# Performance work log

Measured on AMD Instinct MI355X. Metric: run time of the kernel, lower is better.

The kernel has to match this reference:

```python
import jax, jax.numpy as jnp
import numpy as np

RING_SIZE = 4
SEGMENT_LEN = 1024
DILATION_RATE = 2
EPS = 1e-8


def setup_inputs() -> dict:
    key = jax.random.key(0)
    kq, kk, kv = jax.random.split(key, 3)
    shape = (1, 4096, 16, 64)  # (b, n, h, d)
    q = jax.random.normal(kq, shape, dtype=jnp.float32)
    k = jax.random.normal(kk, shape, dtype=jnp.float32)
    v = jax.random.normal(kv, shape, dtype=jnp.float32)
    return {"q": q, "k": k, "v": v}


def _gather_dilated_chunks(k_local, v_local, chunk_size):
    """Replicate the ring loop: rank 0, dist not initialized -> KV chunk is
    always the local chunk; only the dilation offset varies per ring step.
    Returns concatenated dilated K, V of total length ring_size*chunk_size."""
    ks, vs = [], []
    base = jnp.arange(chunk_size)
    for step in range(RING_SIZE):
        chunk_rank = (-step) % RING_SIZE
        chunk_start = chunk_rank * chunk_size
        offset = (chunk_start // SEGMENT_LEN) % DILATION_RATE
        if DILATION_RATE == 1:
            idx = base
        else:
            idx = (base * DILATION_RATE + offset) % chunk_size
        ks.append(k_local[:, idx])
        vs.append(v_local[:, idx])
    return jnp.concatenate(ks, axis=1), jnp.concatenate(vs, axis=1)


def reference(q, k, v):
    b, n, h, d = q.shape
    chunk_size = n // RING_SIZE
    k_local = k[:, :chunk_size]  # rank 0 local chunk
    v_local = v[:, :chunk_size]
    K, V = _gather_dilated_chunks(k_local, v_local, chunk_size)  # (b, n, h, d)

    # Online softmax over ring steps is mathematically a single stable softmax
    # over the concatenation of all chunk scores, with +1e-8 on sum_exp.
    scale = 1.0 / jnp.sqrt(jnp.asarray(d, dtype=q.dtype))
    scores = jnp.einsum("bqhd,bkhd->bhqk", q, K) * scale  # (b, h, n, n)
    m = jnp.max(scores, axis=-1, keepdims=True)
    p = jnp.exp(scores - m)
    denom = jnp.sum(p, axis=-1, keepdims=True) + EPS  # (b, h, q, 1)
    out = jnp.einsum("bhqk,bkhd->bqhd", p, V)  # (b, q, h, d)
    out = out / jnp.transpose(denom, (0, 2, 1, 3))  # -> (b, q, h, 1)
    return out
```

## Files before the change

kernel.cpp:

```cpp
#include <hip/hip_runtime.h>


typedef __attribute__((ext_vector_type(8))) _Float16 f16x8;
typedef __attribute__((ext_vector_type(4))) float    f32x4;

constexpr int HEADS = 16;
constexpr int NQ    = 4096;
constexpr int NK    = 1024;
constexpr int KB    = 64;
constexpr int NT    = NK / KB;
constexpr int NTW   = NT / 2;

constexpr int IMG_K  = 0;
constexpr int IMG_V  = 8192;
constexpr int IMG_SZ = 16384;

__device__ __forceinline__ int swz(int row, int b) {
    return row * 128 + (b ^ ((row & 7) << 4));
}

__global__ __launch_bounds__(256)
void prepass(const float* __restrict__ kg, const float* __restrict__ vg,
             char* __restrict__ ws)
{
    const int kt = blockIdx.x;
    const int h  = blockIdx.y;
    const int kb = kt * KB;
    char* img = ws + (size_t)(h * NT + kt) * IMG_SZ;
    const int tid = threadIdx.x;

    #pragma unroll
    for (int i = 0; i < 2; ++i) {
        int u = i * 256 + tid;
        int f = u >> 6, l = u & 63;
        int t = f >> 1, cc = f & 1;
        int g = l >> 4, c = l & 15;
        const float* src = kg + (size_t)(kb + 16 * t + c) * 1024 + h * 64 + 32 * cc + 8 * g;
        float4 a = *(const float4*)src;
        float4 b = *(const float4*)(src + 4);
        f16x8 kk;
        kk[0] = (_Float16)(a.x * 0.125f); kk[1] = (_Float16)(a.y * 0.125f);
        kk[2] = (_Float16)(a.z * 0.125f); kk[3] = (_Float16)(a.w * 0.125f);
        kk[4] = (_Float16)(b.x * 0.125f); kk[5] = (_Float16)(b.y * 0.125f);
        kk[6] = (_Float16)(b.z * 0.125f); kk[7] = (_Float16)(b.w * 0.125f);
        *(f16x8*)(img + IMG_K + u * 16) = kk;
    }

    #pragma unroll
    for (int i = 0; i < 2; ++i) {
        int u = i * 256 + tid;
        int f = u >> 6, l = u & 63;
        int cc = f >> 2, td = f & 3;
        int g = l >> 4, c = l & 15;
        f16x8 vv;
        #pragma unroll
        for (int e = 0; e < 8; ++e)
            vv[e] = (_Float16)vg[(size_t)(kb + cc * 32 + g * 8 + e) * 1024 + h * 64 + td * 16 + c];
        *(f16x8*)(img + IMG_V + u * 16) = vv;
    }
}

__global__ __launch_bounds__(128, 2)
void ring_attn_v14(const float* __restrict__ qg,
                   const char* __restrict__ ws,
                   float* __restrict__ outg)
{
    __shared__ char  Pl[2][8192];
    __shared__ float Ob[64][64];
    __shared__ float Ls[64];

    const int bid  = blockIdx.x;
    const int xcd  = bid & 7;
    const int slot = bid >> 3;
    const int h    = xcd * 2 + (slot >> 6);
    const int qw   = slot & 63;

    const int tid  = threadIdx.x;
    const int w    = tid >> 6;
    const int lane = tid & 63;
    const int g    = lane >> 4;
    const int c    = lane & 15;
    const int qbase = qw * 64;

    const int rot  = ((bid >> 3) ^ (w << 2)) & 7;

    f16x8 qf[4][2];
    #pragma unroll
    for (int H = 0; H < 4; ++H)
        #pragma unroll
        for (int cc = 0; cc < 2; ++cc) {
            const float* src = qg + (size_t)(qbase + 16 * H + c) * 1024 + h * 64 + 32 * cc + 8 * g;
            float4 a = *(const float4*)src;
            float4 b = *(const float4*)(src + 4);
            f16x8 qq;
            qq[0] = (_Float16)a.x; qq[1] = (_Float16)a.y;
            qq[2] = (_Float16)a.z; qq[3] = (_Float16)a.w;
            qq[4] = (_Float16)b.x; qq[5] = (_Float16)b.y;
            qq[6] = (_Float16)b.z; qq[7] = (_Float16)b.w;
            qf[H][cc] = qq;
        }

    const f32x4 zero4 = {0.f, 0.f, 0.f, 0.f};

    f32x4 o[4][4];
    #pragma unroll
    for (int H = 0; H < 4; ++H)
        #pragma unroll
        for (int td = 0; td < 4; ++td) o[H][td] = zero4;
    float lac[4] = {0.f, 0.f, 0.f, 0.f};

    const char* himg = ws + (size_t)h * NT * IMG_SZ + lane * 16;
    char* pbuf = Pl[w];

    #pragma unroll 1
    for (int i = 0; i < NTW; ++i) {
        const int kt = w * NTW + ((i + rot) & 7);
        const char* img = himg + (size_t)kt * IMG_SZ;

        f16x8 kv[8];
        #pragma unroll
        for (int f = 0; f < 8; ++f)
            kv[f] = *(const f16x8*)(img + IMG_K + f * 1024);

        f32x4 s0[4], s1[4], s2[4], s3[4];
        __builtin_amdgcn_s_setprio(1);
        #pragma unroll
        for (int t = 0; t < 4; ++t) {
            s0[t] = __builtin_amdgcn_mfma_f32_16x16x32_f16(kv[2 * t],     qf[0][0], zero4, 0, 0, 0);
            s0[t] = __builtin_amdgcn_mfma_f32_16x16x32_f16(kv[2 * t + 1], qf[0][1], s0[t], 0, 0, 0);
            s1[t] = __builtin_amdgcn_mfma_f32_16x16x32_f16(kv[2 * t],     qf[1][0], zero4, 0, 0, 0);
            s1[t] = __builtin_amdgcn_mfma_f32_16x16x32_f16(kv[2 * t + 1], qf[1][1], s1[t], 0, 0, 0);
        }
        __builtin_amdgcn_s_setprio(0);
        #pragma unroll
        for (int t = 0; t < 4; ++t) {
            float p0 = __builtin_amdgcn_exp2f(fmaf(s0[t][0], 1.44269504f, -2.88539008f));
            float p1 = __builtin_amdgcn_exp2f(fmaf(s0[t][1], 1.44269504f, -2.88539008f));
            float p2 = __builtin_amdgcn_exp2f(fmaf(s0[t][2], 1.44269504f, -2.88539008f));
            float p3 = __builtin_amdgcn_exp2f(fmaf(s0[t][3], 1.44269504f, -2.88539008f));
            lac[0] += (p0 + p1) + (p2 + p3);
            auto lo = __builtin_amdgcn_cvt_pkrtz(p0, p1);
            auto hi = __builtin_amdgcn_cvt_pkrtz(p2, p3);
            uint2 pk;
            pk.x = __builtin_bit_cast(unsigned int, lo);
            pk.y = __builtin_bit_cast(unsigned int, hi);
            *(uint2*)(pbuf + swz(c, 32 * t + 8 * g)) = pk;
        }
        #pragma unroll
        for (int t = 0; t < 4; ++t) {
            float p0 = __builtin_amdgcn_exp2f(fmaf(s1[t][0], 1.44269504f, -2.88539008f));
            float p1 = __builtin_amdgcn_exp2f(fmaf(s1[t][1], 1.44269504f, -2.88539008f));
            float p2 = __builtin_amdgcn_exp2f(fmaf(s1[t][2], 1.44269504f, -2.88539008f));
            float p3 = __builtin_amdgcn_exp2f(fmaf(s1[t][3], 1.44269504f, -2.88539008f));
            lac[1] += (p0 + p1) + (p2 + p3);
            auto lo = __builtin_amdgcn_cvt_pkrtz(p0, p1);
            auto hi = __builtin_amdgcn_cvt_pkrtz(p2, p3);
            uint2 pk;
            pk.x = __builtin_bit_cast(unsigned int, lo);
            pk.y = __builtin_bit_cast(unsigned int, hi);
            *(uint2*)(pbuf + swz(16 + c, 32 * t + 8 * g)) = pk;
        }

        __builtin_amdgcn_s_setprio(1);
        #pragma unroll
        for (int t = 0; t < 4; ++t) {
            s2[t] = __builtin_amdgcn_mfma_f32_16x16x32_f16(kv[2 * t],     qf[2][0], zero4, 0, 0, 0);
            s2[t] = __builtin_amdgcn_mfma_f32_16x16x32_f16(kv[2 * t + 1], qf[2][1], s2[t], 0, 0, 0);
            s3[t] = __builtin_amdgcn_mfma_f32_16x16x32_f16(kv[2 * t],     qf[3][0], zero4, 0, 0, 0);
            s3[t] = __builtin_amdgcn_mfma_f32_16x16x32_f16(kv[2 * t + 1], qf[3][1], s3[t], 0, 0, 0);
        }
        __builtin_amdgcn_s_setprio(0);

        #pragma unroll
        for (int f = 0; f < 8; ++f)
            kv[f] = *(const f16x8*)(img + IMG_V + f * 1024);

        #pragma unroll
        for (int t = 0; t < 4; ++t) {
            float p0 = __builtin_amdgcn_exp2f(fmaf(s2[t][0], 1.44269504f, -2.88539008f));
            float p1 = __builtin_amdgcn_exp2f(fmaf(s2[t][1], 1.44269504f, -2.88539008f));
            float p2 = __builtin_amdgcn_exp2f(fmaf(s2[t][2], 1.44269504f, -2.88539008f));
            float p3 = __builtin_amdgcn_exp2f(fmaf(s2[t][3], 1.44269504f, -2.88539008f));
            lac[2] += (p0 + p1) + (p2 + p3);
            auto lo = __builtin_amdgcn_cvt_pkrtz(p0, p1);
            auto hi = __builtin_amdgcn_cvt_pkrtz(p2, p3);
            uint2 pk;
            pk.x = __builtin_bit_cast(unsigned int, lo);
            pk.y = __builtin_bit_cast(unsigned int, hi);
            *(uint2*)(pbuf + swz(32 + c, 32 * t + 8 * g)) = pk;
        }
        #pragma unroll
        for (int t = 0; t < 4; ++t) {
            float p0 = __builtin_amdgcn_exp2f(fmaf(s3[t][0], 1.44269504f, -2.88539008f));
            float p1 = __builtin_amdgcn_exp2f(fmaf(s3[t][1], 1.44269504f, -2.88539008f));
            float p2 = __builtin_amdgcn_exp2f(fmaf(s3[t][2], 1.44269504f, -2.88539008f));
            float p3 = __builtin_amdgcn_exp2f(fmaf(s3[t][3], 1.44269504f, -2.88539008f));
            lac[3] += (p0 + p1) + (p2 + p3);
            auto lo = __builtin_amdgcn_cvt_pkrtz(p0, p1);
            auto hi = __builtin_amdgcn_cvt_pkrtz(p2, p3);
            uint2 pk;
            pk.x = __builtin_bit_cast(unsigned int, lo);
            pk.y = __builtin_bit_cast(unsigned int, hi);
            *(uint2*)(pbuf + swz(48 + c, 32 * t + 8 * g)) = pk;
        }

        __builtin_amdgcn_s_setprio(1);
        #pragma unroll
        for (int cc = 0; cc < 2; ++cc) {
            #pragma unroll
            for (int H = 0; H < 4; ++H) {
                f16x8 pa = *(const f16x8*)(pbuf + swz(16 * H + c, 64 * cc + 16 * g));
                #pragma unroll
                for (int td = 0; td < 4; ++td)
                    o[H][td] = __builtin_amdgcn_mfma_f32_16x16x32_f16(pa, kv[cc * 4 + td], o[H][td], 0, 0, 0);
            }
        }
        __builtin_amdgcn_s_setprio(0);
        __builtin_amdgcn_sched_barrier(0);
    }

    #pragma unroll
    for (int H = 0; H < 4; ++H) {
        lac[H] += __shfl_xor(lac[H], 16);
        lac[H] += __shfl_xor(lac[H], 32);
    }

    if (w == 1) {
        #pragma unroll
        for (int H = 0; H < 4; ++H)
            #pragma unroll
            for (int td = 0; td < 4; ++td)
                #pragma unroll
                for (int r = 0; r < 4; ++r)
                    Ob[16 * H + 4 * g + r][16 * td + c] = o[H][td][r];
        if (lane < 16) {
            #pragma unroll
            for (int H = 0; H < 4; ++H) Ls[16 * H + lane] = lac[H];
        }
    }
    __syncthreads();

    if (w == 0) {
        #pragma unroll
        for (int H = 0; H < 4; ++H) {
            #pragma unroll
            for (int r = 0; r < 4; ++r) {
                int q2  = 16 * H + 4 * g + r;
                float lq = __shfl(lac[H], 4 * g + r) + Ls[q2];
                float inv = 1.f / lq;
                int qrow = qbase + q2;
                #pragma unroll
                for (int td = 0; td < 4; ++td)
                    outg[(size_t)qrow * 1024 + h * 64 + 16 * td + c] =
                        (o[H][td][r] + Ob[q2][16 * td + c]) * inv;
            }
        }
    }
}

extern "C" void kernel_launch(void* const* d_in, const int* in_sizes, int n_in,
                              void* d_out, int out_size, void* d_ws, size_t ws_size,
                              hipStream_t stream) {
    const float* q = (const float*)d_in[0];
    const float* k = (const float*)d_in[1];
    const float* v = (const float*)d_in[2];
    float* out = (float*)d_out;
    char* ws = (char*)d_ws;

    prepass<<<dim3(NT, HEADS), dim3(256), 0, stream>>>(k, v, ws);
    ring_attn_v14<<<dim3(1024), dim3(128), 0, stream>>>(q, ws, out);
}
```

Measured before the change: 37.20 us.

## Feed P directly from registers into PV MFMA by transposing the product

New measurement: 34.84 us. 6.3% less time.

```diff
diff --git a/kernel.cpp b/kernel.cpp
--- a/kernel.cpp
+++ b/kernel.cpp
@@ -3,6 +3,7 @@
 
 typedef __attribute__((ext_vector_type(8))) _Float16 f16x8;
 typedef __attribute__((ext_vector_type(4))) float    f32x4;
+typedef __attribute__((ext_vector_type(4))) int      i32x4;
 
 constexpr int HEADS = 16;
 constexpr int NQ    = 4096;
@@ -50,24 +51,24 @@
     for (int i = 0; i < 2; ++i) {
         int u = i * 256 + tid;
         int f = u >> 6, l = u & 63;
-        int cc = f >> 2, td = f & 3;
+        int m = f >> 2, td = f & 3;
         int g = l >> 4, c = l & 15;
         f16x8 vv;
         #pragma unroll
-        for (int e = 0; e < 8; ++e)
-            vv[e] = (_Float16)vg[(size_t)(kb + cc * 32 + g * 8 + e) * 1024 + h * 64 + td * 16 + c];
+        for (int e = 0; e < 8; ++e) {
+            int key = kb + 32 * m + 16 * (e >> 2) + 4 * g + (e & 3);
+            vv[e] = (_Float16)vg[(size_t)key * 1024 + h * 64 + 16 * td + c];
+        }
         *(f16x8*)(img + IMG_V + u * 16) = vv;
     }
 }
 
 __global__ __launch_bounds__(128, 2)
-void ring_attn_v14(const float* __restrict__ qg,
+void ring_attn_v15(const float* __restrict__ qg,
                    const char* __restrict__ ws,
                    float* __restrict__ outg)
 {
-    __shared__ char  Pl[2][8192];
-    __shared__ float Ob[64][64];
-    __shared__ float Ls[64];
+    __shared__ __align__(16) float Ob[64 * 68 + 64];
 
     const int bid  = blockIdx.x;
     const int xcd  = bid & 7;
@@ -110,7 +111,6 @@
     float lac[4] = {0.f, 0.f, 0.f, 0.f};
 
     const char* himg = ws + (size_t)h * NT * IMG_SZ + lane * 16;
-    char* pbuf = Pl[w];
 
     #pragma unroll 1
     for (int i = 0; i < NTW; ++i) {
@@ -123,6 +123,7 @@
             kv[f] = *(const f16x8*)(img + IMG_K + f * 1024);
 
         f32x4 s0[4], s1[4], s2[4], s3[4];
+        unsigned int wv[4][4][2];
         __builtin_amdgcn_s_setprio(1);
         #pragma unroll
         for (int t = 0; t < 4; ++t) {
@@ -139,12 +140,8 @@
             float p2 = __builtin_amdgcn_exp2f(fmaf(s0[t][2], 1.44269504f, -2.88539008f));
             float p3 = __builtin_amdgcn_exp2f(fmaf(s0[t][3], 1.44269504f, -2.88539008f));
             lac[0] += (p0 + p1) + (p2 + p3);
-            auto lo = __builtin_amdgcn_cvt_pkrtz(p0, p1);
-            auto hi = __builtin_amdgcn_cvt_pkrtz(p2, p3);
-            uint2 pk;
-            pk.x = __builtin_bit_cast(unsigned int, lo);
-            pk.y = __builtin_bit_cast(unsigned int, hi);
-            *(uint2*)(pbuf + swz(c, 32 * t + 8 * g)) = pk;
+            wv[0][t][0] = __builtin_bit_cast(unsigned int, __builtin_amdgcn_cvt_pkrtz(p0, p1));
+            wv[0][t][1] = __builtin_bit_cast(unsigned int, __builtin_amdgcn_cvt_pkrtz(p2, p3));
         }
         #pragma unroll
         for (int t = 0; t < 4; ++t) {
@@ -153,12 +150,8 @@
             float p2 = __builtin_amdgcn_exp2f(fmaf(s1[t][2], 1.44269504f, -2.88539008f));
             float p3 = __builtin_amdgcn_exp2f(fmaf(s1[t][3], 1.44269504f, -2.88539008f));
             lac[1] += (p0 + p1) + (p2 + p3);
-            auto lo = __builtin_amdgcn_cvt_pkrtz(p0, p1);
-            auto hi = __builtin_amdgcn_cvt_pkrtz(p2, p3);
-            uint2 pk;
-            pk.x = __builtin_bit_cast(unsigned int, lo);
-            pk.y = __builtin_bit_cast(unsigned int, hi);
-            *(uint2*)(pbuf + swz(16 + c, 32 * t + 8 * g)) = pk;
+            wv[1][t][0] = __builtin_bit_cast(unsigned int, __builtin_amdgcn_cvt_pkrtz(p0, p1));
+            wv[1][t][1] = __builtin_bit_cast(unsigned int, __builtin_amdgcn_cvt_pkrtz(p2, p3));
         }
 
         __builtin_amdgcn_s_setprio(1);
@@ -182,12 +175,8 @@
             float p2 = __builtin_amdgcn_exp2f(fmaf(s2[t][2], 1.44269504f, -2.88539008f));
             float p3 = __builtin_amdgcn_exp2f(fmaf(s2[t][3], 1.44269504f, -2.88539008f));
             lac[2] += (p0 + p1) + (p2 + p3);
-            auto lo = __builtin_amdgcn_cvt_pkrtz(p0, p1);
-            auto hi = __builtin_amdgcn_cvt_pkrtz(p2, p3);
-            uint2 pk;
-            pk.x = __builtin_bit_cast(unsigned int, lo);
-            pk.y = __builtin_bit_cast(unsigned int, hi);
-            *(uint2*)(pbuf + swz(32 + c, 32 * t + 8 * g)) = pk;
+            wv[2][t][0] = __builtin_bit_cast(unsigned int, __builtin_amdgcn_cvt_pkrtz(p0, p1));
+            wv[2][t][1] = __builtin_bit_cast(unsigned int, __builtin_amdgcn_cvt_pkrtz(p2, p3));
         }
         #pragma unroll
         for (int t = 0; t < 4; ++t) {
@@ -196,23 +185,24 @@
             float p2 = __builtin_amdgcn_exp2f(fmaf(s3[t][2], 1.44269504f, -2.88539008f));
             float p3 = __builtin_amdgcn_exp2f(fmaf(s3[t][3], 1.44269504f, -2.88539008f));
             lac[3] += (p0 + p1) + (p2 + p3);
-            auto lo = __builtin_amdgcn_cvt_pkrtz(p0, p1);
-            auto hi = __builtin_amdgcn_cvt_pkrtz(p2, p3);
-            uint2 pk;
-            pk.x = __builtin_bit_cast(unsigned int, lo);
-            pk.y = __builtin_bit_cast(unsigned int, hi);
-            *(uint2*)(pbuf + swz(48 + c, 32 * t + 8 * g)) = pk;
+            wv[3][t][0] = __builtin_bit_cast(unsigned int, __builtin_amdgcn_cvt_pkrtz(p0, p1));
+            wv[3][t][1] = __builtin_bit_cast(unsigned int, __builtin_amdgcn_cvt_pkrtz(p2, p3));
         }
 
         __builtin_amdgcn_s_setprio(1);
         #pragma unroll
-        for (int cc = 0; cc < 2; ++cc) {
-            #pragma unroll
-            for (int H = 0; H < 4; ++H) {
-                f16x8 pa = *(const f16x8*)(pbuf + swz(16 * H + c, 64 * cc + 16 * g));
-                #pragma unroll
-                for (int td = 0; td < 4; ++td)
-                    o[H][td] = __builtin_amdgcn_mfma_f32_16x16x32_f16(pa, kv[cc * 4 + td], o[H][td], 0, 0, 0);
+        for (int H = 0; H < 4; ++H) {
+            i32x4 c0, c1;
+            c0[0] = wv[H][0][0]; c0[1] = wv[H][0][1];
+            c0[2] = wv[H][1][0]; c0[3] = wv[H][1][1];
+            c1[0] = wv[H][2][0]; c1[1] = wv[H][2][1];
+            c1[2] = wv[H][3][0]; c1[3] = wv[H][3][1];
+            f16x8 B0 = __builtin_bit_cast(f16x8, c0);
+            f16x8 B1 = __builtin_bit_cast(f16x8, c1);
+            #pragma unroll
+            for (int td = 0; td < 4; ++td) {
+                o[H][td] = __builtin_amdgcn_mfma_f32_16x16x32_f16(kv[td],     B0, o[H][td], 0, 0, 0);
+                o[H][td] = __builtin_amdgcn_mfma_f32_16x16x32_f16(kv[4 + td], B1, o[H][td], 0, 0, 0);
             }
         }
         __builtin_amdgcn_s_setprio(0);
@@ -225,14 +215,17 @@
         lac[H] += __shfl_xor(lac[H], 32);
     }
 
+    float* Ls = Ob + 64 * 68;
     if (w == 1) {
         #pragma unroll
         for (int H = 0; H < 4; ++H)
             #pragma unroll
-            for (int td = 0; td < 4; ++td)
-                #pragma unroll
-                for (int r = 0; r < 4; ++r)
-                    Ob[16 * H + 4 * g + r][16 * td + c] = o[H][td][r];
+            for (int td = 0; td < 4; ++td) {
+                float4 st;
+                st.x = o[H][td][0]; st.y = o[H][td][1];
+                st.z = o[H][td][2]; st.w = o[H][td][3];
+                *(float4*)&Ob[(16 * H + c) * 68 + 16 * td + 4 * g] = st;
+            }
         if (lane < 16) {
             #pragma unroll
             for (int H = 0; H < 4; ++H) Ls[16 * H + lane] = lac[H];
@@ -243,16 +236,16 @@
     if (w == 0) {
         #pragma unroll
         for (int H = 0; H < 4; ++H) {
-            #pragma unroll
-            for (int r = 0; r < 4; ++r) {
-                int q2  = 16 * H + 4 * g + r;
-                float lq = __shfl(lac[H], 4 * g + r) + Ls[q2];
-                float inv = 1.f / lq;
-                int qrow = qbase + q2;
-                #pragma unroll
-                for (int td = 0; td < 4; ++td)
-                    outg[(size_t)qrow * 1024 + h * 64 + 16 * td + c] =
-                        (o[H][td][r] + Ob[q2][16 * td + c]) * inv;
+            float inv = 1.f / (lac[H] + Ls[16 * H + c]);
+            #pragma unroll
+            for (int td = 0; td < 4; ++td) {
+                float4 pb = *(const float4*)&Ob[(16 * H + c) * 68 + 16 * td + 4 * g];
+                float4 st;
+                st.x = (o[H][td][0] + pb.x) * inv;
+                st.y = (o[H][td][1] + pb.y) * inv;
+                st.z = (o[H][td][2] + pb.z) * inv;
+                st.w = (o[H][td][3] + pb.w) * inv;
+                *(float4*)(outg + (size_t)(qbase + 16 * H + c) * 1024 + h * 64 + 16 * td + 4 * g) = st;
             }
         }
     }
@@ -268,5 +261,5 @@
     char* ws = (char*)d_ws;
 
     prepass<<<dim3(NT, HEADS), dim3(256), 0, stream>>>(k, v, ws);
-    ring_attn_v14<<<dim3(1024), dim3(128), 0, stream>>>(q, ws, out);
-}
+    ring_attn_v15<<<dim3(1024), dim3(128), 0, stream>>>(q, ws, out);
+}
```
